# Kernel tuning notes

Hardware: AMD Instinct MI355X
Metric: run time of the kernel (lower is better)

Reference implementation:

```python
import jax, jax.numpy as jnp
import numpy as np

B, DIM, H = 64, 768, 12
WH, WW = 14, 14
N = WH * WW + 1  # 197
HD = DIM // H    # 64
NUM_REL = (2 * WH - 1) * (2 * WW - 1) + 3  # 732


def _relative_position_index(wh, ww):
    coords = np.stack(np.meshgrid(np.arange(wh), np.arange(ww), indexing='ij'))  # [2,wh,ww]
    flat = coords.reshape(2, -1)                                                # [2, wh*ww]
    rel = flat[:, :, None] - flat[:, None, :]                                   # [2, M, M]
    rel = rel.transpose(1, 2, 0).astype(np.int64)                               # [M, M, 2]
    rel[:, :, 0] += wh - 1
    rel[:, :, 1] += ww - 1
    rel[:, :, 0] *= 2 * ww - 1
    nrd = (2 * wh - 1) * (2 * ww - 1) + 3
    m = wh * ww
    idx = np.zeros((m + 1, m + 1), dtype=np.int32)
    idx[1:, 1:] = rel.sum(-1)
    idx[0, :] = nrd - 3
    idx[:, 0] = nrd - 2
    idx[0, 0] = nrd - 1
    return idx


def setup_inputs() -> dict:
    key = jax.random.key(0)
    ks = jax.random.split(key, 7)
    x = jax.random.normal(ks[0], (B, N, DIM), dtype=jnp.float32)
    Wqkv = jax.random.normal(ks[1], (3 * DIM, DIM), dtype=jnp.float32) * 0.02
    q_bias = jax.random.normal(ks[2], (DIM,), dtype=jnp.float32) * 0.02
    v_bias = jax.random.normal(ks[3], (DIM,), dtype=jnp.float32) * 0.02
    rel_table = jax.random.normal(ks[4], (NUM_REL, H), dtype=jnp.float32) * 0.02
    Wproj = jax.random.normal(ks[5], (DIM, DIM), dtype=jnp.float32) * 0.02
    bproj = jax.random.normal(ks[6], (DIM,), dtype=jnp.float32) * 0.02
    rel_index = jnp.asarray(_relative_position_index(WH, WW))  # [N, N] int32
    return {"x": x, "Wqkv": Wqkv, "q_bias": q_bias, "v_bias": v_bias,
            "rel_table": rel_table, "Wproj": Wproj, "bproj": bproj,
            "rel_index": rel_index}


def reference(x, Wqkv, q_bias, v_bias, rel_table, Wproj, bproj, rel_index):
    b, n, c = x.shape
    hd = Wqkv.shape[0] // (3 * H)
    scale = hd ** -0.5
    qkv_bias = jnp.concatenate([q_bias, jnp.zeros_like(v_bias), v_bias])
    qkv = x @ Wqkv.T + qkv_bias                              # [B,N,3*DIM]
    qkv = qkv.reshape(b, n, 3, H, hd).transpose(2, 0, 3, 1, 4)  # [3,B,H,N,hd]
    q, k, v = qkv[0] * scale, qkv[1], qkv[2]
    attn = jnp.einsum('bhqd,bhkd->bhqk', q, k)               # [B,H,N,N]
    rel_bias = rel_table[rel_index].transpose(2, 0, 1)       # [H,N,N]
    attn = jax.nn.softmax(attn + rel_bias[None], axis=-1)
    out = jnp.einsum('bhqk,bhkd->bhqd', attn, v)             # [B,H,N,hd]
    out = out.transpose(0, 2, 1, 3).reshape(b, n, -1)        # [B,N,DIM]
    return out @ Wproj.T + bproj
```

## Files before the change

### kernel.cpp

```cpp
#include <hip/hip_runtime.h>

typedef _Float16 f16_t;
typedef f16_t f16x8 __attribute__((ext_vector_type(8)));
typedef float f32x4 __attribute__((ext_vector_type(4)));

#define DEVI __device__ __forceinline__

constexpr int NB    = 64;
constexpr int NTOK  = 197;
constexpr int NH    = 12;
constexpr int DIM   = 768;
constexpr int M_TOK = NB * NTOK;
constexpr int NPAD  = 224;
constexpr float SCALE = 0.125f;

constexpr int KP_SZ  = 2 * NPAD * 32;
constexpr int VTS_SZ = 7 * 64 * 32;
constexpr int P_LD   = 228;
constexpr int PW_SZ  = 16 * P_LD;
constexpr int ATTN_LDS = (KP_SZ + VTS_SZ + 8 * PW_SZ) * 2;

DEVI ushort f2h_bits(float f) { _Float16 h = (_Float16)f; return __builtin_bit_cast(ushort, h); }

DEVI void gload16(const void* g, void* l) {
    __builtin_amdgcn_global_load_lds((const __attribute__((address_space(1))) void*)g,
                                     (__attribute__((address_space(3))) void*)l, 16, 0, 0);
}

DEVI int xcd_swz(int orig, int nwg) {
    const int q = nwg >> 3, r = nwg & 7;
    const int xcd = orig & 7, idx = orig >> 3;
    return (xcd < r ? xcd * (q + 1) : r * (q + 1) + (xcd - r) * q) + idx;
}

__global__ __launch_bounds__(256) void k_cvt3(const float* __restrict__ s0, ushort* __restrict__ d0, int n0,
                                              const float* __restrict__ s1, ushort* __restrict__ d1, int n1,
                                              const float* __restrict__ s2, ushort* __restrict__ d2, int n2) {
    int i = blockIdx.x * 256 + threadIdx.x;
    const float* s; ushort* d;
    if (i < n0)           { s = s0; d = d0; }
    else if (i < n0 + n1) { i -= n0; s = s1; d = d1; }
    else                  { i -= n0 + n1; if (i >= n2) return; s = s2; d = d2; }
    float4 v = reinterpret_cast<const float4*>(s)[i];
    ushort4 o;
    o.x = f2h_bits(v.x); o.y = f2h_bits(v.y); o.z = f2h_bits(v.z); o.w = f2h_bits(v.w);
    reinterpret_cast<ushort4*>(d)[i] = o;
}

__global__ __launch_bounds__(256) void k_bias(const float* __restrict__ rel_table,
                                              const int* __restrict__ rel_index,
                                              ushort* __restrict__ biash) {
    int idx = blockIdx.x * 256 + threadIdx.x;
    if (idx >= NH * NPAD * 256) return;
    const int j  = idx & 15;
    const int fr = (idx >> 4) & 15;
    const int i  = (idx >> 8) % NPAD;
    const int h  = (idx >> 8) / NPAD;
    const int col = j * 16 + fr;
    float v = -30000.f;
    if (i < NTOK && col < NTOK && j < 14) v = rel_table[rel_index[i * NTOK + col] * NH + h];
    biash[idx] = f2h_bits(v);
}

__global__ __launch_bounds__(512, 2) void k_qkv8(const ushort* __restrict__ A, const ushort* __restrict__ BT,
                                                 const float* __restrict__ b_q, const float* __restrict__ b_v,
                                                 ushort* __restrict__ outp) {
    constexpr int M = M_TOK, N = 2304, K = 768, nt = K / 64;
    constexpr int NWG = (N / 256) * 50;
    extern __shared__ ushort lds[];
    ushort* ldsA = lds;
    ushort* ldsB = lds + 32768;
    const int tid = threadIdx.x, wid = tid >> 6, lane = tid & 63;
    const int wm = wid >> 2, wn = wid & 3;
    const int fr = lane & 15, fg = lane >> 4;
    const int bid = xcd_swz(blockIdx.y * (N / 256) + blockIdx.x, NWG);
    const int m0 = (bid / (N / 256)) * 256, n0 = (bid % (N / 256)) * 256;

    const int srow = tid >> 2;
    const int sc = ((tid & 3) ^ ((tid >> 3) & 3)) * 8;
    int ra0 = m0 + srow;       ra0 = ra0 < M ? ra0 : M - 1;
    int ra1 = m0 + srow + 128; ra1 = ra1 < M ? ra1 : M - 1;
    const ushort* pA0 = A + (size_t)ra0 * K + sc;
    const ushort* pA1 = A + (size_t)ra1 * K + sc;
    const ushort* pB0 = BT + (size_t)(n0 + srow) * K + sc;
    const ushort* pB1 = BT + (size_t)(n0 + srow + 128) * K + sc;
    const int dstt = tid * 8;

    int aoff[8], boff[4];
#pragma unroll
    for (int mi = 0; mi < 8; ++mi) {
        const int r = wm * 128 + mi * 16 + fr;
        aoff[mi] = r * 32 + ((fg ^ ((r >> 1) & 3)) * 8);
    }
#pragma unroll
    for (int j = 0; j < 4; ++j) {
        const int c = wn * 64 + j * 16 + fr;
        boff[j] = c * 32 + ((fg ^ ((c >> 1) & 3)) * 8);
    }

    f32x4 acc[8][4] = {};
    f16x8 av[8];

    auto STAGE = [&](int T, int isA, int k) {
        const int Tw = T >= nt ? T - nt : T;
        const size_t so = (size_t)(Tw * 64 + k * 32);
        const int db = (T & 1) * 16384 + k * 8192 + dstt;
        if (isA) { gload16(pA0 + so, ldsA + db); gload16(pA1 + so, ldsA + db + 4096); }
        else     { gload16(pB0 + so, ldsB + db); gload16(pB1 + so, ldsB + db + 4096); }
    };

#define LDA8(B_, KS_) { _Pragma("unroll") for (int mi = 0; mi < 8; ++mi) \
        av[mi] = *(const f16x8*)(ldsA + (B_) * 16384 + (KS_) * 8192 + aoff[mi]); }

#define PHASE(B_, KS_, NH_, LA_, ST_T, ST_A, ST_K, GATE_) { \
        if (LA_) LDA8(B_, KS_); \
        f16x8 bv0 = *(const f16x8*)(ldsB + (B_) * 16384 + (KS_) * 8192 + boff[(NH_) * 2]); \
        f16x8 bv1 = *(const f16x8*)(ldsB + (B_) * 16384 + (KS_) * 8192 + boff[(NH_) * 2 + 1]); \
        STAGE(ST_T, ST_A, ST_K); \
        __builtin_amdgcn_s_barrier(); \
        __builtin_amdgcn_s_setprio(1); \
        _Pragma("unroll") for (int mi = 0; mi < 8; ++mi) { \
            acc[mi][(NH_) * 2]     = __builtin_amdgcn_mfma_f32_16x16x32_f16(av[mi], bv0, acc[mi][(NH_) * 2], 0, 0, 0); \
            acc[mi][(NH_) * 2 + 1] = __builtin_amdgcn_mfma_f32_16x16x32_f16(av[mi], bv1, acc[mi][(NH_) * 2 + 1], 0, 0, 0); } \
        __builtin_amdgcn_s_setprio(0); \
        asm volatile("s_waitcnt lgkmcnt(0)" ::: "memory"); \
        __builtin_amdgcn_sched_barrier(0); \
        if (GATE_) { asm volatile("s_waitcnt vmcnt(4)" ::: "memory"); __builtin_amdgcn_sched_barrier(0); } \
        __builtin_amdgcn_s_barrier(); }

    STAGE(0, 1, 0); STAGE(0, 0, 0); STAGE(0, 1, 1); STAGE(0, 0, 1);
    STAGE(1, 1, 0); STAGE(1, 0, 0);
    asm volatile("s_waitcnt vmcnt(4)" ::: "memory");
    __builtin_amdgcn_sched_barrier(0);
    __builtin_amdgcn_s_barrier();

    for (int i = 0; i < nt / 2; ++i) {
        const int t0 = 2 * i;
        PHASE(0, 0, 0, 1, t0 + 1, 1, 1, 0)
        PHASE(0, 0, 1, 0, t0 + 1, 0, 1, 0)
        PHASE(0, 1, 0, 1, t0 + 2, 1, 0, 0)
        PHASE(0, 1, 1, 0, t0 + 2, 0, 0, 1)
        PHASE(1, 0, 0, 1, t0 + 2, 1, 1, 0)
        PHASE(1, 0, 1, 0, t0 + 2, 0, 1, 0)
        PHASE(1, 1, 0, 1, t0 + 3, 1, 0, 0)
        PHASE(1, 1, 1, 0, t0 + 3, 0, 0, 1)
    }
#undef PHASE
#undef LDA8

    asm volatile("s_waitcnt vmcnt(0) lgkmcnt(0)" ::: "memory");
    __builtin_amdgcn_sched_barrier(0);
    __builtin_amdgcn_s_barrier();

    ushort* ws = lds + wid * 8192;
#pragma unroll
    for (int ni = 0; ni < 4; ++ni) {
        const int col = n0 + wn * 64 + ni * 16 + fr;
        float addv, mul;
        if (col < 768)       { addv = b_q[col]; mul = SCALE; }
        else if (col < 1536) { addv = 0.f; mul = 1.f; }
        else                 { addv = b_v[col - 1536]; mul = 1.f; }
#pragma unroll
        for (int mi = 0; mi < 8; ++mi)
#pragma unroll
            for (int r = 0; r < 4; ++r)
                ws[(mi * 16 + fg * 4 + r) * 64 + ni * 16 + fr] = f2h_bits((acc[mi][ni][r] + addv) * mul);
    }
    __syncthreads();
#pragma unroll
    for (int it = 0; it < 16; ++it) {
        const int g = it * 64 + lane;
        const int r = g >> 3, seg = g & 7;
        const int row = m0 + wm * 128 + r;
        uint4 v = *(const uint4*)(ws + r * 64 + seg * 8);
        if (row < M) *(uint4*)(outp + (size_t)row * N + n0 + wn * 64 + seg * 8) = v;
    }
}

template<int EPI>
__global__ __launch_bounds__(256) void k_gemm(const ushort* __restrict__ A, const ushort* __restrict__ BT,
                                              int M, int N, int K, int nwg,
                                              const float* __restrict__ b_q, const float* __restrict__ b_v,
                                              const float* __restrict__ b_p,
                                              ushort* __restrict__ out_h, float* __restrict__ out_f) {
    __shared__ __align__(16) ushort lds[2][8192];
    const int tid = threadIdx.x, wid = tid >> 6, lane = tid & 63;
    const int wm = wid >> 1, wn = wid & 1;
    const int fr = lane & 15, fg = lane >> 4;
    const int nbx = N / 128;
    const int bid = xcd_swz(blockIdx.y * nbx + blockIdx.x, nwg);
    const int m0 = (bid / nbx) * 128, n0 = (bid % nbx) * 128;

    int rA[2], rB[2], cs[2], dst[2];
#pragma unroll
    for (int i = 0; i < 2; ++i) {
        const int g = (wid * 2 + i) * 64 + lane;
        const int row = g >> 2, sp = g & 3;
        cs[i]  = (sp ^ ((row >> 1) & 3)) * 8;
        dst[i] = (wid * 2 + i) * 512;
        const int ra = m0 + row;
        rA[i] = ra < M ? ra : M - 1;
        rB[i] = n0 + row;
    }

    f32x4 acc[4][4] = {};
    const int nt = K / 32;

    auto stage = [&](int t, int buf) {
#pragma unroll
        for (int i = 0; i < 2; ++i)
            gload16(A + (size_t)rA[i] * K + t * 32 + cs[i], &lds[buf][dst[i]]);
#pragma unroll
        for (int i = 0; i < 2; ++i)
            gload16(BT + (size_t)rB[i] * K + t * 32 + cs[i], &lds[buf][4096 + dst[i]]);
    };

    stage(0, 0);
    __syncthreads();
    for (int t = 0; t < nt; ++t) {
        const int cur = t & 1;
        if (t + 1 < nt) stage(t + 1, cur ^ 1);
        const ushort* As = lds[cur];
        const ushort* Bs = lds[cur] + 4096;
        f16x8 af[4], bf[4];
#pragma unroll
        for (int i = 0; i < 4; ++i) {
            const int r = wm * 64 + i * 16 + fr;
            af[i] = *(const f16x8*)(As + r * 32 + ((fg ^ ((r >> 1) & 3)) * 8));
        }
#pragma unroll
        for (int i = 0; i < 4; ++i) {
            const int c = wn * 64 + i * 16 + fr;
            bf[i] = *(const f16x8*)(Bs + c * 32 + ((fg ^ ((c >> 1) & 3)) * 8));
        }
#pragma unroll
        for (int mi = 0; mi < 4; ++mi)
#pragma unroll
            for (int ni = 0; ni < 4; ++ni)
                acc[mi][ni] = __builtin_amdgcn_mfma_f32_16x16x32_f16(af[mi], bf[ni], acc[mi][ni], 0, 0, 0);
        __syncthreads();
    }

#pragma unroll
    for (int ni = 0; ni < 4; ++ni) {
        const int col = n0 + wn * 64 + ni * 16 + fr;
        float addv = 0.f, mul = 1.f;
        if (EPI == 0) {
            if (col < 768)       { addv = b_q[col]; mul = SCALE; }
            else if (col < 1536) { addv = 0.f; }
            else                 { addv = b_v[col - 1536]; }
        } else {
            addv = b_p[col];
        }
#pragma unroll
        for (int mi = 0; mi < 4; ++mi) {
#pragma unroll
            for (int r = 0; r < 4; ++r) {
                const int row = m0 + wm * 64 + mi * 16 + fg * 4 + r;
                if (row < M) {
                    float v = (acc[mi][ni][r] + addv) * mul;
                    if (EPI == 0) out_h[(size_t)row * N + col] = f2h_bits(v);
                    else          out_f[(size_t)row * N + col] = v;
                }
            }
        }
    }
}

__global__ __launch_bounds__(512) void k_attn(const ushort* __restrict__ qkv,
                                              const ushort* __restrict__ biash, ushort* __restrict__ out) {
    extern __shared__ ushort sm[];
    ushort* kp  = sm;
    ushort* vts = sm + KP_SZ;
    ushort* ps  = sm + KP_SZ + VTS_SZ;
    const int tid = threadIdx.x, wid = tid >> 6, lane = tid & 63;
    const int fr = lane & 15, fg = lane >> 4;
    const int bh = blockIdx.x;
    const int b = bh / NH, h = bh % NH;
    const size_t qb = (size_t)(b * NTOK) * 2304;
    const int swz8 = (fg ^ ((fr >> 1) & 3)) * 8;

    ushort* vtile = ps;
    for (int t = tid; t < NPAD * 8; t += 512) {
        const int row = t >> 3, seg = t & 7;
        uint4 kv = make_uint4(0u, 0u, 0u, 0u), vv = make_uint4(0u, 0u, 0u, 0u);
        if (row < NTOK) {
            const ushort* src = qkv + qb + (size_t)row * 2304 + 768 + h * 64;
            kv = *reinterpret_cast<const uint4*>(src + seg * 8);
            vv = *reinterpret_cast<const uint4*>(src + 768 + seg * 8);
        }
        const int pcg = (seg & 3) ^ ((row >> 1) & 3);
        *reinterpret_cast<uint4*>(kp + (seg >> 2) * (NPAD * 32) + row * 32 + pcg * 8) = kv;
        *reinterpret_cast<uint4*>(vtile + row * 72 + seg * 8) = vv;
    }
    __syncthreads();
    for (int o = tid; o < 7 * 64 * 4; o += 512) {
        const int kc = o >> 8, rem = o & 255, d = rem >> 2, pcg = rem & 3;
        const int k0 = kc * 32 + (pcg ^ ((d >> 1) & 3)) * 8;
        ushort w[8];
#pragma unroll
        for (int e = 0; e < 8; ++e) w[e] = vtile[(k0 + e) * 72 + d];
        uint4 val;
        val.x = (uint)w[0] | ((uint)w[1] << 16);
        val.y = (uint)w[2] | ((uint)w[3] << 16);
        val.z = (uint)w[4] | ((uint)w[5] << 16);
        val.w = (uint)w[6] | ((uint)w[7] << 16);
        *reinterpret_cast<uint4*>(vts + kc * 2048 + d * 32 + pcg * 8) = val;
    }
    __syncthreads();

    ushort* pw = ps + wid * PW_SZ;

    for (int s = wid; s < 13; s += 8) {
        const int q0 = s * 16;
        f16x8 qf[2];
        {
            int row = q0 + fr;
            row = row < NTOK ? row : NTOK - 1;
            const ushort* qp = qkv + qb + (size_t)row * 2304 + h * 64 + fg * 8;
            qf[0] = *reinterpret_cast<const f16x8*>(qp);
            qf[1] = *reinterpret_cast<const f16x8*>(qp + 32);
        }
        f32x4 sacc[14] = {};
#pragma unroll
        for (int j = 0; j < 14; ++j) {
#pragma unroll
            for (int kh = 0; kh < 2; ++kh) {
                f16x8 kf = *reinterpret_cast<const f16x8*>(kp + kh * (NPAD * 32) + (j * 16 + fr) * 32 + swz8);
                sacc[j] = __builtin_amdgcn_mfma_f32_16x16x32_f16(qf[kh], kf, sacc[j], 0, 0, 0);
            }
        }
        float rs4[4];
#pragma unroll
        for (int r = 0; r < 4; ++r) {
            const int qrow_l = fg * 4 + r;
            int qrow = q0 + qrow_l;
            qrow = qrow < NTOK ? qrow : NTOK - 1;
            const ushort* bp16 = biash + (((size_t)(h * NPAD + qrow) * 16 + fr) << 4);
            f16x8 bv0 = *reinterpret_cast<const f16x8*>(bp16);
            f16x8 bv1 = *reinterpret_cast<const f16x8*>(bp16 + 8);
            float mx = -1e30f;
#pragma unroll
            for (int j = 0; j < 14; ++j) {
                const float bj = (float)(j < 8 ? bv0[j] : bv1[j - 8]);
                float v = sacc[j][r] + bj;
                sacc[j][r] = v;
                mx = fmaxf(mx, v);
            }
            mx = fmaxf(mx, __shfl_xor(mx, 1));
            mx = fmaxf(mx, __shfl_xor(mx, 2));
            mx = fmaxf(mx, __shfl_xor(mx, 4));
            mx = fmaxf(mx, __shfl_xor(mx, 8));
            float sum = 0.f;
            ushort* prow = pw + qrow_l * P_LD;
#pragma unroll
            for (int j = 0; j < 14; ++j) {
                float p = __expf(sacc[j][r] - mx);
                sum += p;
                prow[j * 16 + fr] = f2h_bits(p);
            }
            sum += __shfl_xor(sum, 1);
            sum += __shfl_xor(sum, 2);
            sum += __shfl_xor(sum, 4);
            sum += __shfl_xor(sum, 8);
            rs4[r] = sum;
        }
        f32x4 o[4] = {};
#pragma unroll
        for (int kc = 0; kc < 7; ++kc) {
            f16x8 af = *reinterpret_cast<const f16x8*>(pw + fr * P_LD + kc * 32 + fg * 8);
#pragma unroll
            for (int dt = 0; dt < 4; ++dt) {
                f16x8 bv = *reinterpret_cast<const f16x8*>(vts + kc * 2048 + (dt * 16 + fr) * 32 + swz8);
                o[dt] = __builtin_amdgcn_mfma_f32_16x16x32_f16(af, bv, o[dt], 0, 0, 0);
            }
        }
#pragma unroll
        for (int dt = 0; dt < 4; ++dt) {
#pragma unroll
            for (int r = 0; r < 4; ++r) {
                const int qrow = q0 + fg * 4 + r;
                if (qrow < NTOK) {
                    const float val = o[dt][r] / rs4[r];
                    out[(size_t)(b * NTOK + qrow) * DIM + h * 64 + dt * 16 + fr] = f2h_bits(val);
                }
            }
        }
    }
}

extern "C" void kernel_launch(void* const* d_in, const int* in_sizes, int n_in,
                              void* d_out, int out_size, void* d_ws, size_t ws_size,
                              hipStream_t stream) {
    const float* x         = (const float*)d_in[0];
    const float* Wqkv      = (const float*)d_in[1];
    const float* q_bias    = (const float*)d_in[2];
    const float* v_bias    = (const float*)d_in[3];
    const float* rel_table = (const float*)d_in[4];
    const float* Wproj     = (const float*)d_in[5];
    const float* bproj     = (const float*)d_in[6];
    const int*   rel_index = (const int*)d_in[7];
    float* out = (float*)d_out;

    char* p = (char*)d_ws;
    auto alloc = [&](size_t bytes) { char* r = p; p += (bytes + 255) & ~(size_t)255; return r; };
    ushort* xb     = (ushort*)alloc((size_t)M_TOK * DIM * 2);
    ushort* wqkvb  = (ushort*)alloc((size_t)2304 * 768 * 2);
    ushort* wprojb = (ushort*)alloc((size_t)768 * 768 * 2);
    ushort* qkvb   = (ushort*)alloc((size_t)M_TOK * 2304 * 2);
    ushort* biasb  = (ushort*)alloc((size_t)NH * NPAD * 256 * 2);
    ushort* aob    = (ushort*)alloc((size_t)M_TOK * DIM * 2);

    (void)hipFuncSetAttribute((const void*)k_qkv8, hipFuncAttributeMaxDynamicSharedMemorySize, 131072);
    (void)hipFuncSetAttribute((const void*)k_attn, hipFuncAttributeMaxDynamicSharedMemorySize, ATTN_LDS);

    const int n0 = M_TOK * DIM / 4, n1 = 2304 * 768 / 4, n2 = 768 * 768 / 4;
    k_cvt3<<<(n0 + n1 + n2 + 255) / 256, 256, 0, stream>>>(x, xb, n0, Wqkv, wqkvb, n1, Wproj, wprojb, n2);
    int nbias = NH * NPAD * 256;
    k_bias<<<(nbias + 255) / 256, 256, 0, stream>>>(rel_table, rel_index, biasb);

    k_qkv8<<<dim3(2304 / 256, (M_TOK + 255) / 256), 512, 131072, stream>>>(
        xb, wqkvb, q_bias, v_bias, qkvb);
    k_attn<<<dim3(NB * NH), 512, ATTN_LDS, stream>>>(qkvb, biasb, aob);
    k_gemm<1><<<dim3(768 / 128, (M_TOK + 127) / 128), 256, 0, stream>>>(
        aob, wprojb, M_TOK, 768, 768, (768 / 128) * ((M_TOK + 127) / 128),
        nullptr, nullptr, bproj, nullptr, out);
}
```

Baseline: 154.3 us.

## Halve QKV GEMM LDS footprint for higher occupancy and merge prep kernels

The QKV GEMM now stages 32-wide K tiles in a simple double buffer (64KB LDS instead of 128KB), with launch bounds raised so more workgroups can share a CU. The finer-grained 8-phase software pipeline becomes a plain loop that waits for all loads every iteration. The epilogue is split into two halves to fit the smaller LDS. Separately, the conversion and bias-table kernels are merged into one launch to save a kernel dispatch. The trade is more occupancy against less load/compute overlap per workgroup and higher register pressure from the tighter launch bound.

```diff
diff --git a/kernel.cpp b/kernel.cpp
--- a/kernel.cpp
+++ b/kernel.cpp
@@ -33,43 +33,45 @@
     return (xcd < r ? xcd * (q + 1) : r * (q + 1) + (xcd - r) * q) + idx;
 }
 
-__global__ __launch_bounds__(256) void k_cvt3(const float* __restrict__ s0, ushort* __restrict__ d0, int n0,
-                                              const float* __restrict__ s1, ushort* __restrict__ d1, int n1,
-                                              const float* __restrict__ s2, ushort* __restrict__ d2, int n2) {
-    int i = blockIdx.x * 256 + threadIdx.x;
-    const float* s; ushort* d;
-    if (i < n0)           { s = s0; d = d0; }
-    else if (i < n0 + n1) { i -= n0; s = s1; d = d1; }
-    else                  { i -= n0 + n1; if (i >= n2) return; s = s2; d = d2; }
-    float4 v = reinterpret_cast<const float4*>(s)[i];
-    ushort4 o;
-    o.x = f2h_bits(v.x); o.y = f2h_bits(v.y); o.z = f2h_bits(v.z); o.w = f2h_bits(v.w);
-    reinterpret_cast<ushort4*>(d)[i] = o;
-}
-
-__global__ __launch_bounds__(256) void k_bias(const float* __restrict__ rel_table,
-                                              const int* __restrict__ rel_index,
-                                              ushort* __restrict__ biash) {
-    int idx = blockIdx.x * 256 + threadIdx.x;
-    if (idx >= NH * NPAD * 256) return;
-    const int j  = idx & 15;
-    const int fr = (idx >> 4) & 15;
-    const int i  = (idx >> 8) % NPAD;
-    const int h  = (idx >> 8) / NPAD;
-    const int col = j * 16 + fr;
-    float v = -30000.f;
-    if (i < NTOK && col < NTOK && j < 14) v = rel_table[rel_index[i * NTOK + col] * NH + h];
-    biash[idx] = f2h_bits(v);
-}
-
-__global__ __launch_bounds__(512, 2) void k_qkv8(const ushort* __restrict__ A, const ushort* __restrict__ BT,
+__global__ __launch_bounds__(256) void k_pre(const float* __restrict__ s0, ushort* __restrict__ d0, int n0,
+                                             const float* __restrict__ s1, ushort* __restrict__ d1, int n1,
+                                             const float* __restrict__ s2, ushort* __restrict__ d2, int n2,
+                                             int ncvtblk,
+                                             const float* __restrict__ rel_table,
+                                             const int* __restrict__ rel_index,
+                                             ushort* __restrict__ biash) {
+    if ((int)blockIdx.x < ncvtblk) {
+        int i = blockIdx.x * 256 + threadIdx.x;
+        const float* s; ushort* d;
+        if (i < n0)           { s = s0; d = d0; }
+        else if (i < n0 + n1) { i -= n0; s = s1; d = d1; }
+        else                  { i -= n0 + n1; if (i >= n2) return; s = s2; d = d2; }
+        float4 v = reinterpret_cast<const float4*>(s)[i];
+        ushort4 o;
+        o.x = f2h_bits(v.x); o.y = f2h_bits(v.y); o.z = f2h_bits(v.z); o.w = f2h_bits(v.w);
+        reinterpret_cast<ushort4*>(d)[i] = o;
+    } else {
+        int idx = (blockIdx.x - ncvtblk) * 256 + threadIdx.x;
+        if (idx >= NH * NPAD * 256) return;
+        const int j  = idx & 15;
+        const int fr = (idx >> 4) & 15;
+        const int i  = (idx >> 8) % NPAD;
+        const int h  = (idx >> 8) / NPAD;
+        const int col = j * 16 + fr;
+        float v = -30000.f;
+        if (i < NTOK && col < NTOK && j < 14) v = rel_table[rel_index[i * NTOK + col] * NH + h];
+        biash[idx] = f2h_bits(v);
+    }
+}
+
+__global__ __launch_bounds__(512, 4) void k_qkv8(const ushort* __restrict__ A, const ushort* __restrict__ BT,
                                                  const float* __restrict__ b_q, const float* __restrict__ b_v,
                                                  ushort* __restrict__ outp) {
-    constexpr int M = M_TOK, N = 2304, K = 768, nt = K / 64;
+    constexpr int M = M_TOK, N = 2304, K = 768, nt = K / 32;
     constexpr int NWG = (N / 256) * 50;
     extern __shared__ ushort lds[];
     ushort* ldsA = lds;
-    ushort* ldsB = lds + 32768;
+    ushort* ldsB = lds + 16384;
     const int tid = threadIdx.x, wid = tid >> 6, lane = tid & 63;
     const int wm = wid >> 2, wn = wid & 3;
     const int fr = lane & 15, fg = lane >> 4;
@@ -101,79 +103,81 @@
     f32x4 acc[8][4] = {};
     f16x8 av[8];
 
-    auto STAGE = [&](int T, int isA, int k) {
-        const int Tw = T >= nt ? T - nt : T;
-        const size_t so = (size_t)(Tw * 64 + k * 32);
-        const int db = (T & 1) * 16384 + k * 8192 + dstt;
-        if (isA) { gload16(pA0 + so, ldsA + db); gload16(pA1 + so, ldsA + db + 4096); }
-        else     { gload16(pB0 + so, ldsB + db); gload16(pB1 + so, ldsB + db + 4096); }
+    auto STAGE = [&](int t) {
+        const size_t so = (size_t)t * 32;
+        const int db = (t & 1) * 8192 + dstt;
+        gload16(pA0 + so, ldsA + db);
+        gload16(pA1 + so, ldsA + db + 4096);
+        gload16(pB0 + so, ldsB + db);
+        gload16(pB1 + so, ldsB + db + 4096);
     };
 
-#define LDA8(B_, KS_) { _Pragma("unroll") for (int mi = 0; mi < 8; ++mi) \
-        av[mi] = *(const f16x8*)(ldsA + (B_) * 16384 + (KS_) * 8192 + aoff[mi]); }
-
-#define PHASE(B_, KS_, NH_, LA_, ST_T, ST_A, ST_K, GATE_) { \
-        if (LA_) LDA8(B_, KS_); \
-        f16x8 bv0 = *(const f16x8*)(ldsB + (B_) * 16384 + (KS_) * 8192 + boff[(NH_) * 2]); \
-        f16x8 bv1 = *(const f16x8*)(ldsB + (B_) * 16384 + (KS_) * 8192 + boff[(NH_) * 2 + 1]); \
-        STAGE(ST_T, ST_A, ST_K); \
-        __builtin_amdgcn_s_barrier(); \
-        __builtin_amdgcn_s_setprio(1); \
-        _Pragma("unroll") for (int mi = 0; mi < 8; ++mi) { \
-            acc[mi][(NH_) * 2]     = __builtin_amdgcn_mfma_f32_16x16x32_f16(av[mi], bv0, acc[mi][(NH_) * 2], 0, 0, 0); \
-            acc[mi][(NH_) * 2 + 1] = __builtin_amdgcn_mfma_f32_16x16x32_f16(av[mi], bv1, acc[mi][(NH_) * 2 + 1], 0, 0, 0); } \
-        __builtin_amdgcn_s_setprio(0); \
-        asm volatile("s_waitcnt lgkmcnt(0)" ::: "memory"); \
-        __builtin_amdgcn_sched_barrier(0); \
-        if (GATE_) { asm volatile("s_waitcnt vmcnt(4)" ::: "memory"); __builtin_amdgcn_sched_barrier(0); } \
-        __builtin_amdgcn_s_barrier(); }
-
-    STAGE(0, 1, 0); STAGE(0, 0, 0); STAGE(0, 1, 1); STAGE(0, 0, 1);
-    STAGE(1, 1, 0); STAGE(1, 0, 0);
-    asm volatile("s_waitcnt vmcnt(4)" ::: "memory");
+    STAGE(0);
+    asm volatile("s_waitcnt vmcnt(0)" ::: "memory");
     __builtin_amdgcn_sched_barrier(0);
     __builtin_amdgcn_s_barrier();
 
-    for (int i = 0; i < nt / 2; ++i) {
-        const int t0 = 2 * i;
-        PHASE(0, 0, 0, 1, t0 + 1, 1, 1, 0)
-        PHASE(0, 0, 1, 0, t0 + 1, 0, 1, 0)
-        PHASE(0, 1, 0, 1, t0 + 2, 1, 0, 0)
-        PHASE(0, 1, 1, 0, t0 + 2, 0, 0, 1)
-        PHASE(1, 0, 0, 1, t0 + 2, 1, 1, 0)
-        PHASE(1, 0, 1, 0, t0 + 2, 0, 1, 0)
-        PHASE(1, 1, 0, 1, t0 + 3, 1, 0, 0)
-        PHASE(1, 1, 1, 0, t0 + 3, 0, 0, 1)
-    }
-#undef PHASE
-#undef LDA8
-
-    asm volatile("s_waitcnt vmcnt(0) lgkmcnt(0)" ::: "memory");
-    __builtin_amdgcn_sched_barrier(0);
-    __builtin_amdgcn_s_barrier();
-
-    ushort* ws = lds + wid * 8192;
-#pragma unroll
-    for (int ni = 0; ni < 4; ++ni) {
-        const int col = n0 + wn * 64 + ni * 16 + fr;
-        float addv, mul;
-        if (col < 768)       { addv = b_q[col]; mul = SCALE; }
-        else if (col < 1536) { addv = 0.f; mul = 1.f; }
-        else                 { addv = b_v[col - 1536]; mul = 1.f; }
+    for (int t = 0; t < nt; ++t) {
+        const int buf = t & 1;
+        if (t + 1 < nt) STAGE(t + 1);
 #pragma unroll
         for (int mi = 0; mi < 8; ++mi)
-#pragma unroll
-            for (int r = 0; r < 4; ++r)
-                ws[(mi * 16 + fg * 4 + r) * 64 + ni * 16 + fr] = f2h_bits((acc[mi][ni][r] + addv) * mul);
-    }
-    __syncthreads();
-#pragma unroll
-    for (int it = 0; it < 16; ++it) {
-        const int g = it * 64 + lane;
-        const int r = g >> 3, seg = g & 7;
-        const int row = m0 + wm * 128 + r;
-        uint4 v = *(const uint4*)(ws + r * 64 + seg * 8);
-        if (row < M) *(uint4*)(outp + (size_t)row * N + n0 + wn * 64 + seg * 8) = v;
+            av[mi] = *(const f16x8*)(ldsA + buf * 8192 + aoff[mi]);
+        f16x8 bv0 = *(const f16x8*)(ldsB + buf * 8192 + boff[0]);
+        f16x8 bv1 = *(const f16x8*)(ldsB + buf * 8192 + boff[1]);
+        __builtin_amdgcn_s_barrier();
+        __builtin_amdgcn_s_setprio(1);
+#pragma unroll
+        for (int mi = 0; mi < 8; ++mi) {
+            acc[mi][0] = __builtin_amdgcn_mfma_f32_16x16x32_f16(av[mi], bv0, acc[mi][0], 0, 0, 0);
+            acc[mi][1] = __builtin_amdgcn_mfma_f32_16x16x32_f16(av[mi], bv1, acc[mi][1], 0, 0, 0);
+        }
+        __builtin_amdgcn_s_setprio(0);
+        __builtin_amdgcn_s_barrier();
+        f16x8 bv2 = *(const f16x8*)(ldsB + buf * 8192 + boff[2]);
+        f16x8 bv3 = *(const f16x8*)(ldsB + buf * 8192 + boff[3]);
+        __builtin_amdgcn_s_setprio(1);
+#pragma unroll
+        for (int mi = 0; mi < 8; ++mi) {
+            acc[mi][2] = __builtin_amdgcn_mfma_f32_16x16x32_f16(av[mi], bv2, acc[mi][2], 0, 0, 0);
+            acc[mi][3] = __builtin_amdgcn_mfma_f32_16x16x32_f16(av[mi], bv3, acc[mi][3], 0, 0, 0);
+        }
+        __builtin_amdgcn_s_setprio(0);
+        asm volatile("s_waitcnt lgkmcnt(0)" ::: "memory");
+        __builtin_amdgcn_sched_barrier(0);
+        asm volatile("s_waitcnt vmcnt(0)" ::: "memory");
+        __builtin_amdgcn_sched_barrier(0);
+        __builtin_amdgcn_s_barrier();
+    }
+
+    ushort* ws = lds + wid * 4096;
+#pragma unroll
+    for (int half = 0; half < 2; ++half) {
+#pragma unroll
+        for (int ni = 0; ni < 4; ++ni) {
+            const int col = n0 + wn * 64 + ni * 16 + fr;
+            float addv, mul;
+            if (col < 768)       { addv = b_q[col]; mul = SCALE; }
+            else if (col < 1536) { addv = 0.f; mul = 1.f; }
+            else                 { addv = b_v[col - 1536]; mul = 1.f; }
+#pragma unroll
+            for (int mi2 = 0; mi2 < 4; ++mi2) {
+                const int mi = half * 4 + mi2;
+#pragma unroll
+                for (int r = 0; r < 4; ++r)
+                    ws[(mi2 * 16 + fg * 4 + r) * 64 + ni * 16 + fr] = f2h_bits((acc[mi][ni][r] + addv) * mul);
+            }
+        }
+        __syncthreads();
+#pragma unroll
+        for (int it = 0; it < 8; ++it) {
+            const int g = it * 64 + lane;
+            const int r = g >> 3, seg = g & 7;
+            const int row = m0 + wm * 128 + half * 64 + r;
+            uint4 v = *(const uint4*)(ws + r * 64 + seg * 8);
+            if (row < M) *(uint4*)(outp + (size_t)row * N + n0 + wn * 64 + seg * 8) = v;
+        }
+        __syncthreads();
     }
 }
 
@@ -411,15 +415,16 @@
     ushort* biasb  = (ushort*)alloc((size_t)NH * NPAD * 256 * 2);
     ushort* aob    = (ushort*)alloc((size_t)M_TOK * DIM * 2);
 
-    (void)hipFuncSetAttribute((const void*)k_qkv8, hipFuncAttributeMaxDynamicSharedMemorySize, 131072);
+    (void)hipFuncSetAttribute((const void*)k_qkv8, hipFuncAttributeMaxDynamicSharedMemorySize, 65536);
     (void)hipFuncSetAttribute((const void*)k_attn, hipFuncAttributeMaxDynamicSharedMemorySize, ATTN_LDS);
 
     const int n0 = M_TOK * DIM / 4, n1 = 2304 * 768 / 4, n2 = 768 * 768 / 4;
-    k_cvt3<<<(n0 + n1 + n2 + 255) / 256, 256, 0, stream>>>(x, xb, n0, Wqkv, wqkvb, n1, Wproj, wprojb, n2);
-    int nbias = NH * NPAD * 256;
-    k_bias<<<(nbias + 255) / 256, 256, 0, stream>>>(rel_table, rel_index, biasb);
-
-    k_qkv8<<<dim3(2304 / 256, (M_TOK + 255) / 256), 512, 131072, stream>>>(
+    const int ncvtblk = (n0 + n1 + n2 + 255) / 256;
+    const int nbiasblk = (NH * NPAD * 256 + 255) / 256;
+    k_pre<<<ncvtblk + nbiasblk, 256, 0, stream>>>(x, xb, n0, Wqkv, wqkvb, n1, Wproj, wprojb, n2,
+                                                  ncvtblk, rel_table, rel_index, biasb);
+
+    k_qkv8<<<dim3(2304 / 256, (M_TOK + 255) / 256), 512, 65536, stream>>>(
         xb, wqkvb, q_bias, v_bias, qkvb);
     k_attn<<<dim3(NB * NH), 512, ATTN_LDS, stream>>>(qkvb, biasb, aob);
     k_gemm<1><<<dim3(768 / 128, (M_TOK + 127) / 128), 256, 0, stream>>>(
```

Result: slower. 466.0 us (+202.0%).
